# Optimization experiments

Measured on AMD Instinct MI355X. Metric: run time of the kernel, lower is better.

## Reference

```python
import jax, jax.numpy as jnp
import numpy as np

B, S, D, H = 4, 1024, 1024, 16
DK = D // H
NEG = -1e9


def setup_inputs() -> dict:
    key = jax.random.key(0)
    ks = jax.random.split(key, 14)
    sc = 1.0 / np.sqrt(D)
    inp = {
        "query": jax.random.normal(ks[0], (B, S, D), jnp.float32),
        "key": jax.random.normal(ks[1], (B, S, D), jnp.float32),
        "value": jax.random.normal(ks[2], (B, S, D), jnp.float32),
        "mask": jax.random.randint(ks[3], (B, S, S), 0, 2, jnp.int32),
        "group_prob": jax.random.uniform(ks[4], (B, S, S), jnp.float32),
        "Wq": jax.random.normal(ks[5], (D, D), jnp.float32) * sc,
        "bq": jnp.zeros((D,), jnp.float32),
        "Wk": jax.random.normal(ks[6], (D, D), jnp.float32) * sc,
        "bk": jnp.zeros((D,), jnp.float32),
        "Wv": jax.random.normal(ks[7], (D, D), jnp.float32) * sc,
        "bv": jnp.zeros((D,), jnp.float32),
        "Wo": jax.random.normal(ks[8], (D, D), jnp.float32) * sc,
        "bo": jnp.zeros((D,), jnp.float32),
    }
    return inp


def reference(query, key, value, mask, group_prob, Wq, bq, Wk, bk, Wv, bv, Wo, bo):
    # QKV projections, split heads: [B,S,D] -> [B,H,S,DK]
    def proj(x, W, b):
        return (x @ W.T + b).reshape(B, S, H, DK).transpose(0, 2, 1, 3)

    q = proj(query, Wq, bq)
    k = proj(key, Wk, bk)
    v = proj(value, Wv, bv)

    scores = jnp.einsum("bhqd,bhkd->bhqk", q, k) / jnp.sqrt(jnp.float32(DK))

    # group_prob branch: allowed where mask OR diagonal is nonzero
    diag = jnp.eye(S, dtype=jnp.int32)
    allowed = (mask[:, None, :, :] | diag[None, None, :, :]) != 0  # [B,1,S,S]
    scores = jnp.where(allowed, scores, NEG)

    p_attn = jax.nn.softmax(scores, axis=-1)
    p_attn = p_attn * group_prob[:, None, :, :]  # post-softmax group reweighting

    x = jnp.einsum("bhqk,bhkd->bhqd", p_attn, v)
    x = x.transpose(0, 2, 1, 3).reshape(B, S, D)
    return x @ Wo.T + bo
```

## Files before the change

kernel.cpp:

```cpp
#include <hip/hip_runtime.h>
#include <hip/hip_bf16.h>


typedef __attribute__((ext_vector_type(8))) __bf16 bf16x8;
typedef __attribute__((ext_vector_type(4))) float f32x4;
typedef __attribute__((ext_vector_type(8))) unsigned short u16x8;

#define GSTR 40

__device__ __forceinline__ bf16x8 lds_read8(const unsigned short* p) {
  bf16x8 r;
  __builtin_memcpy(&r, __builtin_assume_aligned(p, 16), 16);
  return r;
}
__device__ __forceinline__ void lds_write8(unsigned short* p, const void* v) {
  __builtin_memcpy(__builtin_assume_aligned(p, 16), v, 16);
}
__device__ __forceinline__ u16x8 cvt8h(const float4 a, const float4 b) {
  const float fv[8] = {a.x, a.y, a.z, a.w, b.x, b.y, b.z, b.w};
  union { u16x8 v; __bf16 e[8]; } hh;
#pragma unroll
  for (int i = 0; i < 8; ++i) hh.e[i] = (__bf16)fv[i];
  return hh.v;
}
__device__ __forceinline__ void cvt8hl(const float4 a, const float4 b, u16x8* hi, u16x8* lo) {
  const float fv[8] = {a.x, a.y, a.z, a.w, b.x, b.y, b.z, b.w};
  union { u16x8 v; __bf16 e[8]; } hh, ll;
#pragma unroll
  for (int i = 0; i < 8; ++i) {
    const __bf16 h = (__bf16)fv[i];
    hh.e[i] = h;
    ll.e[i] = (__bf16)(fv[i] - (float)h);
  }
  *hi = hh.v; *lo = ll.v;
}
__device__ __forceinline__ unsigned short bfbits(float f) {
  const __bf16 h = (__bf16)f;
  unsigned short u; __builtin_memcpy(&u, &h, 2); return u;
}

__global__ __launch_bounds__(256) void k_gemm_qkv(
    const float* __restrict__ X0, const float* __restrict__ X1, const float* __restrict__ X2,
    const float* __restrict__ W0, const float* __restrict__ W1, const float* __restrict__ W2,
    const float* __restrict__ B0, const float* __restrict__ B1, const float* __restrict__ B2,
    float* __restrict__ O0, float* __restrict__ O1, float* __restrict__ O2)
{
  const int z = blockIdx.z;
  const float* X = (z == 0) ? X0 : (z == 1) ? X1 : X2;
  const float* W = (z == 0) ? W0 : (z == 1) ? W1 : W2;
  const float* Bi = (z == 0) ? B0 : (z == 1) ? B1 : B2;
  float* O = (z == 0) ? O0 : (z == 1) ? O1 : O2;

  const int bid = blockIdx.x;
  const int swz = (bid & 7) * 64 + (bid >> 3);
  const int n0 = (swz & 15) * 64, m0 = (swz >> 4) * 128;

  __shared__ alignas(16) unsigned short Ah[128 * GSTR];
  __shared__ alignas(16) unsigned short Bh[64 * GSTR];
  const int tid = threadIdx.x, l = tid & 63, w = tid >> 6;
  const int wr = w >> 1, wc = w & 1;

  f32x4 acc[4][2];
#pragma unroll
  for (int i = 0; i < 4; ++i)
#pragma unroll
    for (int j = 0; j < 2; ++j) acc[i][j] = (f32x4){0.f, 0.f, 0.f, 0.f};

  const int arow = tid >> 1, ac0 = (tid & 1) * 16;
  const int brow = tid >> 2, bc0 = (tid & 3) * 8;
  const float* xsrc = X + (size_t)(m0 + arow) * 1024 + ac0;
  const float* wsrc = W + (size_t)(n0 + brow) * 1024 + bc0;

  float4 fx[4], fw[2];
#pragma unroll
  for (int i = 0; i < 4; ++i) fx[i] = *(const float4*)(xsrc + i * 4);
#pragma unroll
  for (int i = 0; i < 2; ++i) fw[i] = *(const float4*)(wsrc + i * 4);

  for (int kt = 0; kt < 32; ++kt) {
    u16x8 xh[2], wh1;
    xh[0] = cvt8h(fx[0], fx[1]);
    xh[1] = cvt8h(fx[2], fx[3]);
    wh1 = cvt8h(fw[0], fw[1]);
    if (kt < 31) {
      const float* nx = xsrc + (kt + 1) * 32;
      const float* nw = wsrc + (kt + 1) * 32;
#pragma unroll
      for (int i = 0; i < 4; ++i) fx[i] = *(const float4*)(nx + i * 4);
#pragma unroll
      for (int i = 0; i < 2; ++i) fw[i] = *(const float4*)(nw + i * 4);
    }
    __syncthreads();
    lds_write8(&Ah[arow * GSTR + ac0], &xh[0]);
    lds_write8(&Ah[arow * GSTR + ac0 + 8], &xh[1]);
    lds_write8(&Bh[brow * GSTR + bc0], &wh1);
    __syncthreads();

    bf16x8 ah[4], bh[2];
#pragma unroll
    for (int mf = 0; mf < 4; ++mf) {
      const int r = wr * 64 + mf * 16 + (l & 15);
      ah[mf] = lds_read8(&Ah[r * GSTR + (l >> 4) * 8]);
    }
#pragma unroll
    for (int nf = 0; nf < 2; ++nf) {
      const int r = wc * 32 + nf * 16 + (l & 15);
      bh[nf] = lds_read8(&Bh[r * GSTR + (l >> 4) * 8]);
    }
#pragma unroll
    for (int mf = 0; mf < 4; ++mf)
#pragma unroll
      for (int nf = 0; nf < 2; ++nf)
        acc[mf][nf] = __builtin_amdgcn_mfma_f32_16x16x32_bf16(ah[mf], bh[nf], acc[mf][nf], 0, 0, 0);
  }

#pragma unroll
  for (int nf = 0; nf < 2; ++nf) {
    const int col = n0 + wc * 32 + nf * 16 + (l & 15);
    const float bias = Bi[col];
#pragma unroll
    for (int mf = 0; mf < 4; ++mf) {
      const int rbase = m0 + wr * 64 + mf * 16 + (l >> 4) * 4;
#pragma unroll
      for (int j = 0; j < 4; ++j)
        O[(size_t)(rbase + j) * 1024 + col] = acc[mf][nf][j] + bias;
    }
  }
}

__global__ __launch_bounds__(256) void k_gemm_out(
    const float* __restrict__ X, const float* __restrict__ W,
    const float* __restrict__ Bi, float* __restrict__ Out)
{
  const int bid = blockIdx.x;
  const int swz = (bid & 7) * 128 + (bid >> 3);
  const int n0 = (swz & 15) * 64, m0 = (swz >> 4) * 64;

  __shared__ alignas(16) unsigned short Ah[64 * GSTR];
  __shared__ alignas(16) unsigned short Bh[64 * GSTR], Bl[64 * GSTR];
  const int tid = threadIdx.x, l = tid & 63, w = tid >> 6;
  const int wr = w >> 1, wc = w & 1;

  f32x4 acc[2][2];
#pragma unroll
  for (int i = 0; i < 2; ++i)
#pragma unroll
    for (int j = 0; j < 2; ++j) acc[i][j] = (f32x4){0.f, 0.f, 0.f, 0.f};

  const int srow = tid >> 2, sc0 = (tid & 3) * 8;
  const float* xsrc = X + (size_t)(m0 + srow) * 1024 + sc0;
  const float* wsrc = W + (size_t)(n0 + srow) * 1024 + sc0;

  float4 fx[2], fw[2];
#pragma unroll
  for (int i = 0; i < 2; ++i) {
    fx[i] = *(const float4*)(xsrc + i * 4);
    fw[i] = *(const float4*)(wsrc + i * 4);
  }

  for (int kt = 0; kt < 32; ++kt) {
    u16x8 xh, wh1, wl1;
    xh = cvt8h(fx[0], fx[1]);
    cvt8hl(fw[0], fw[1], &wh1, &wl1);
    if (kt < 31) {
      const float* nx = xsrc + (kt + 1) * 32;
      const float* nw = wsrc + (kt + 1) * 32;
#pragma unroll
      for (int i = 0; i < 2; ++i) {
        fx[i] = *(const float4*)(nx + i * 4);
        fw[i] = *(const float4*)(nw + i * 4);
      }
    }
    __syncthreads();
    lds_write8(&Ah[srow * GSTR + sc0], &xh);
    lds_write8(&Bh[srow * GSTR + sc0], &wh1);
    lds_write8(&Bl[srow * GSTR + sc0], &wl1);
    __syncthreads();

    bf16x8 ah[2], bh[2], bl[2];
#pragma unroll
    for (int mf = 0; mf < 2; ++mf) {
      const int r = wr * 32 + mf * 16 + (l & 15);
      ah[mf] = lds_read8(&Ah[r * GSTR + (l >> 4) * 8]);
    }
#pragma unroll
    for (int nf = 0; nf < 2; ++nf) {
      const int r = wc * 32 + nf * 16 + (l & 15);
      bh[nf] = lds_read8(&Bh[r * GSTR + (l >> 4) * 8]);
      bl[nf] = lds_read8(&Bl[r * GSTR + (l >> 4) * 8]);
    }
#pragma unroll
    for (int mf = 0; mf < 2; ++mf)
#pragma unroll
      for (int nf = 0; nf < 2; ++nf) {
        acc[mf][nf] = __builtin_amdgcn_mfma_f32_16x16x32_bf16(ah[mf], bh[nf], acc[mf][nf], 0, 0, 0);
        acc[mf][nf] = __builtin_amdgcn_mfma_f32_16x16x32_bf16(ah[mf], bl[nf], acc[mf][nf], 0, 0, 0);
      }
  }

#pragma unroll
  for (int nf = 0; nf < 2; ++nf) {
    const int col = n0 + wc * 32 + nf * 16 + (l & 15);
    const float bias = Bi[col];
#pragma unroll
    for (int mf = 0; mf < 2; ++mf) {
      const int rbase = m0 + wr * 32 + mf * 16 + (l >> 4) * 4;
#pragma unroll
      for (int j = 0; j < 4; ++j)
        Out[(size_t)(rbase + j) * 1024 + col] = acc[mf][nf][j] + bias;
    }
  }
}

__global__ __launch_bounds__(256) void k_attn(
    const float* Qp, const float* __restrict__ Kp, const float* __restrict__ Vp,
    const int* __restrict__ Mask, const float* __restrict__ Gp,
    float* Xo)
{
  const int h = blockIdx.x, qt = blockIdx.y, b = blockIdx.z;
  __shared__ alignas(16) unsigned short Kh[64 * 64], Vh[64 * 64], Ph[64 * 64];
  const int tid = threadIdx.x, l = tid & 63, w = tid >> 6;

  const float* kbase = Kp + (size_t)b * 1048576 + h * 64;
  const float* vbase = Vp + (size_t)b * 1048576 + h * 64;

  bf16x8 aq[2];
  {
    const int qrow = qt * 64 + w * 16 + (l & 15);
    const float* qp_ = Qp + ((size_t)(b * 1024 + qrow)) * 1024 + h * 64;
#pragma unroll
    for (int ks = 0; ks < 2; ++ks) {
      const float4 t0 = *(const float4*)(qp_ + ks * 32 + (l >> 4) * 8);
      const float4 t1 = *(const float4*)(qp_ + ks * 32 + (l >> 4) * 8 + 4);
      aq[ks] = (bf16x8)cvt8h(t0, t1);
    }
  }

  f32x4 accO[4];
#pragma unroll
  for (int nf = 0; nf < 4; ++nf) accO[nf] = (f32x4){0.f, 0.f, 0.f, 0.f};
  float zacc[4] = {0.f, 0.f, 0.f, 0.f};

  const int qloc0 = w * 16 + (l >> 4) * 4;
  const int qg0 = qt * 64 + qloc0;
  const int mcol = l & 15;

  const int krow = tid >> 2, kd0 = (tid & 3) * 16;
  const int kb4 = (tid & 15) * 4, db4 = (tid >> 4) * 4;

  float4 kreg[4], vreg[4];
  {
    const float* ks_ = kbase + (size_t)krow * 1024 + kd0;
#pragma unroll
    for (int i = 0; i < 4; ++i) kreg[i] = *(const float4*)(ks_ + i * 4);
    const float* vs_ = vbase + (size_t)kb4 * 1024 + db4;
#pragma unroll
    for (int i = 0; i < 4; ++i) vreg[i] = *(const float4*)(vs_ + (size_t)i * 1024);
  }

  for (int kt = 0; kt < 16; ++kt) {
    __syncthreads();

    int mk[4][4]; float gv[4][4];
#pragma unroll
    for (int nf = 0; nf < 4; ++nf) {
      const int kg = kt * 64 + nf * 16 + mcol;
#pragma unroll
      for (int j = 0; j < 4; ++j) {
        const size_t roff = ((size_t)(b * 1024 + qg0 + j)) << 10;
        mk[nf][j] = Mask[roff + kg];
        gv[nf][j] = Gp[roff + kg];
      }
    }

    {
      u16x8 h0 = cvt8h(kreg[0], kreg[1]);
      u16x8 h1 = cvt8h(kreg[2], kreg[3]);
      const int c0 = kd0 ^ ((krow & 7) << 3);
      const int c1 = (kd0 + 8) ^ ((krow & 7) << 3);
      lds_write8(&Kh[krow * 64 + c0], &h0);
      lds_write8(&Kh[krow * 64 + c1], &h1);
    }
    {
      const float col[4][4] = {{vreg[0].x, vreg[1].x, vreg[2].x, vreg[3].x},
                               {vreg[0].y, vreg[1].y, vreg[2].y, vreg[3].y},
                               {vreg[0].z, vreg[1].z, vreg[2].z, vreg[3].z},
                               {vreg[0].w, vreg[1].w, vreg[2].w, vreg[3].w}};
#pragma unroll
      for (int i = 0; i < 4; ++i) {
        const int d = db4 + i;
        union { __bf16 e[4]; unsigned long long v; } pk;
#pragma unroll
        for (int u = 0; u < 4; ++u) pk.e[u] = (__bf16)col[i][u];
        const int c = kb4 ^ ((d & 7) << 3);
        __builtin_memcpy(__builtin_assume_aligned(&Vh[d * 64 + c], 8), &pk.v, 8);
      }
    }
    if (kt < 15) {
      const float* ks_ = kbase + (size_t)((kt + 1) * 64 + krow) * 1024 + kd0;
#pragma unroll
      for (int i = 0; i < 4; ++i) kreg[i] = *(const float4*)(ks_ + i * 4);
      const float* vs_ = vbase + (size_t)((kt + 1) * 64 + kb4) * 1024 + db4;
#pragma unroll
      for (int i = 0; i < 4; ++i) vreg[i] = *(const float4*)(vs_ + (size_t)i * 1024);
    }
    __syncthreads();

#pragma unroll
    for (int nf = 0; nf < 4; ++nf) {
      f32x4 sacc = (f32x4){0.f, 0.f, 0.f, 0.f};
      const int kr = nf * 16 + (l & 15);
#pragma unroll
      for (int ks = 0; ks < 2; ++ks) {
        const int c = (ks * 32 + (l >> 4) * 8) ^ ((kr & 7) << 3);
        sacc = __builtin_amdgcn_mfma_f32_16x16x32_bf16(aq[ks], lds_read8(&Kh[kr * 64 + c]), sacc, 0, 0, 0);
      }
      const int kg = kt * 64 + nf * 16 + mcol;
#pragma unroll
      for (int j = 0; j < 4; ++j) {
        const int qg = qg0 + j;
        const int allowed = mk[nf][j] | (qg == kg);
        const float e = allowed ? exp2f(fmaf(sacc[j], 0.18033688f, -17.31234049f)) : 0.f;
        zacc[j] += e;
        const int qloc = qloc0 + j;
        Ph[qloc * 64 + ((nf * 16 + mcol) ^ ((qloc & 7) << 3))] = bfbits(e * gv[nf][j]);
      }
    }
    bf16x8 pah[2];
    {
      const int ar = w * 16 + (l & 15);
#pragma unroll
      for (int ks = 0; ks < 2; ++ks) {
        const int c = (ks * 32 + (l >> 4) * 8) ^ ((ar & 7) << 3);
        pah[ks] = lds_read8(&Ph[ar * 64 + c]);
      }
    }
#pragma unroll
    for (int nf = 0; nf < 4; ++nf) {
      const int dr = nf * 16 + (l & 15);
#pragma unroll
      for (int ks = 0; ks < 2; ++ks) {
        const int c = (ks * 32 + (l >> 4) * 8) ^ ((dr & 7) << 3);
        accO[nf] = __builtin_amdgcn_mfma_f32_16x16x32_bf16(pah[ks], lds_read8(&Vh[dr * 64 + c]), accO[nf], 0, 0, 0);
      }
    }
  }

#pragma unroll
  for (int j = 0; j < 4; ++j) {
#pragma unroll
    for (int off = 1; off < 16; off <<= 1) zacc[j] += __shfl_xor(zacc[j], off, 64);
  }
  float rz[4];
#pragma unroll
  for (int j = 0; j < 4; ++j) rz[j] = 1.f / zacc[j];

#pragma unroll
  for (int nf = 0; nf < 4; ++nf) {
    const int d = nf * 16 + (l & 15);
#pragma unroll
    for (int j = 0; j < 4; ++j) {
      const int qg = qg0 + j;
      Xo[((size_t)(b * 1024 + qg)) * 1024 + h * 64 + d] = accO[nf][j] * rz[j];
    }
  }
}

extern "C" void kernel_launch(void* const* d_in, const int* in_sizes, int n_in,
                              void* d_out, int out_size, void* d_ws, size_t ws_size,
                              hipStream_t stream) {
  const float* query = (const float*)d_in[0];
  const float* key_in = (const float*)d_in[1];
  const float* value = (const float*)d_in[2];
  const int* mask = (const int*)d_in[3];
  const float* gp = (const float*)d_in[4];
  const float* Wq = (const float*)d_in[5];
  const float* bq = (const float*)d_in[6];
  const float* Wk = (const float*)d_in[7];
  const float* bk = (const float*)d_in[8];
  const float* Wv = (const float*)d_in[9];
  const float* bv = (const float*)d_in[10];
  const float* Wo = (const float*)d_in[11];
  const float* bo = (const float*)d_in[12];
  float* out = (float*)d_out;

  float* kp = (float*)d_ws;
  float* vp = kp + 4194304;
  float* qp = vp + 4194304;
  float* xo = qp;

  hipLaunchKernelGGL(k_gemm_qkv, dim3(512, 1, 3), dim3(256), 0, stream,
                     query, key_in, value, Wq, Wk, Wv, bq, bk, bv, qp, kp, vp);
  hipLaunchKernelGGL(k_attn, dim3(16, 16, 4), dim3(256), 0, stream,
                     qp, kp, vp, mask, gp, xo);
  hipLaunchKernelGGL(k_gemm_out, dim3(1024), dim3(256), 0, stream,
                     xo, Wo, bo, out);
}
```

Measured before the change: 196.0 us.

## Store Q/K/V and attention output intermediates as bf16 with async K loads

The QKV projection now writes bf16 instead of fp32, and the attention kernel and output GEMM read bf16 directly. This halves intermediate memory traffic and removes the in-kernel conversions. The attention kernel also double-buffers K tiles in LDS using global_load_lds direct-to-LDS copies and restructures the mask/group-prob loads. The values were already rounded to bf16 before the MFMAs, so accuracy is essentially unchanged, though the attention output X is now stored in bf16.

Measured after the change: 182.1 us. -7.1%, faster.

```diff
diff --git a/kernel.cpp b/kernel.cpp
--- a/kernel.cpp
+++ b/kernel.cpp
@@ -1,6 +1,9 @@
 #include <hip/hip_runtime.h>
 #include <hip/hip_bf16.h>
 
+
+#define AS1q __attribute__((address_space(1)))
+#define AS3q __attribute__((address_space(3)))
 
 typedef __attribute__((ext_vector_type(8))) __bf16 bf16x8;
 typedef __attribute__((ext_vector_type(4))) float f32x4;
@@ -8,6 +11,9 @@
 
 #define GSTR 40
 
+__device__ __forceinline__ void gload_lds16(const void* g, void* l) {
+  __builtin_amdgcn_global_load_lds((const AS1q void*)g, (AS3q void*)l, 16, 0, 0);
+}
 __device__ __forceinline__ bf16x8 lds_read8(const unsigned short* p) {
   bf16x8 r;
   __builtin_memcpy(&r, __builtin_assume_aligned(p, 16), 16);
@@ -43,13 +49,14 @@
     const float* __restrict__ X0, const float* __restrict__ X1, const float* __restrict__ X2,
     const float* __restrict__ W0, const float* __restrict__ W1, const float* __restrict__ W2,
     const float* __restrict__ B0, const float* __restrict__ B1, const float* __restrict__ B2,
-    float* __restrict__ O0, float* __restrict__ O1, float* __restrict__ O2)
+    unsigned short* __restrict__ O0, unsigned short* __restrict__ O1,
+    unsigned short* __restrict__ O2)
 {
   const int z = blockIdx.z;
   const float* X = (z == 0) ? X0 : (z == 1) ? X1 : X2;
   const float* W = (z == 0) ? W0 : (z == 1) ? W1 : W2;
   const float* Bi = (z == 0) ? B0 : (z == 1) ? B1 : B2;
-  float* O = (z == 0) ? O0 : (z == 1) ? O1 : O2;
+  unsigned short* O = (z == 0) ? O0 : (z == 1) ? O1 : O2;
 
   const int bid = blockIdx.x;
   const int swz = (bid & 7) * 64 + (bid >> 3);
@@ -123,13 +130,13 @@
       const int rbase = m0 + wr * 64 + mf * 16 + (l >> 4) * 4;
 #pragma unroll
       for (int j = 0; j < 4; ++j)
-        O[(size_t)(rbase + j) * 1024 + col] = acc[mf][nf][j] + bias;
+        O[(size_t)(rbase + j) * 1024 + col] = bfbits(acc[mf][nf][j] + bias);
     }
   }
 }
 
 __global__ __launch_bounds__(256) void k_gemm_out(
-    const float* __restrict__ X, const float* __restrict__ W,
+    const unsigned short* __restrict__ X, const float* __restrict__ W,
     const float* __restrict__ Bi, float* __restrict__ Out)
 {
   const int bid = blockIdx.x;
@@ -148,31 +155,26 @@
     for (int j = 0; j < 2; ++j) acc[i][j] = (f32x4){0.f, 0.f, 0.f, 0.f};
 
   const int srow = tid >> 2, sc0 = (tid & 3) * 8;
-  const float* xsrc = X + (size_t)(m0 + srow) * 1024 + sc0;
+  const unsigned short* xsrc = X + (size_t)(m0 + srow) * 1024 + sc0;
   const float* wsrc = W + (size_t)(n0 + srow) * 1024 + sc0;
 
-  float4 fx[2], fw[2];
-#pragma unroll
-  for (int i = 0; i < 2; ++i) {
-    fx[i] = *(const float4*)(xsrc + i * 4);
-    fw[i] = *(const float4*)(wsrc + i * 4);
-  }
+  u16x8 xcur = *(const u16x8*)xsrc;
+  float4 fw[2];
+#pragma unroll
+  for (int i = 0; i < 2; ++i) fw[i] = *(const float4*)(wsrc + i * 4);
 
   for (int kt = 0; kt < 32; ++kt) {
-    u16x8 xh, wh1, wl1;
-    xh = cvt8h(fx[0], fx[1]);
+    const u16x8 xstage = xcur;
+    u16x8 wh1, wl1;
     cvt8hl(fw[0], fw[1], &wh1, &wl1);
     if (kt < 31) {
-      const float* nx = xsrc + (kt + 1) * 32;
+      xcur = *(const u16x8*)(xsrc + (kt + 1) * 32);
       const float* nw = wsrc + (kt + 1) * 32;
 #pragma unroll
-      for (int i = 0; i < 2; ++i) {
-        fx[i] = *(const float4*)(nx + i * 4);
-        fw[i] = *(const float4*)(nw + i * 4);
-      }
-    }
-    __syncthreads();
-    lds_write8(&Ah[srow * GSTR + sc0], &xh);
+      for (int i = 0; i < 2; ++i) fw[i] = *(const float4*)(nw + i * 4);
+    }
+    __syncthreads();
+    lds_write8(&Ah[srow * GSTR + sc0], &xstage);
     lds_write8(&Bh[srow * GSTR + sc0], &wh1);
     lds_write8(&Bl[srow * GSTR + sc0], &wl1);
     __syncthreads();
@@ -213,27 +215,26 @@
 }
 
 __global__ __launch_bounds__(256) void k_attn(
-    const float* Qp, const float* __restrict__ Kp, const float* __restrict__ Vp,
+    const unsigned short* Qh, const unsigned short* __restrict__ Kb,
+    const unsigned short* __restrict__ Vb,
     const int* __restrict__ Mask, const float* __restrict__ Gp,
-    float* Xo)
+    unsigned short* Xo)
 {
   const int h = blockIdx.x, qt = blockIdx.y, b = blockIdx.z;
-  __shared__ alignas(16) unsigned short Kh[64 * 64], Vh[64 * 64], Ph[64 * 64];
+  __shared__ alignas(16) unsigned short Kh[2][64 * 64];
+  __shared__ alignas(16) unsigned short Vh[64 * 64];
+  __shared__ alignas(16) unsigned short Ph[64 * 64];
   const int tid = threadIdx.x, l = tid & 63, w = tid >> 6;
 
-  const float* kbase = Kp + (size_t)b * 1048576 + h * 64;
-  const float* vbase = Vp + (size_t)b * 1048576 + h * 64;
+  const unsigned short* kb_ = Kb + (size_t)b * 1048576 + h * 64;
+  const unsigned short* vb_ = Vb + (size_t)b * 1048576 + h * 64;
 
   bf16x8 aq[2];
   {
     const int qrow = qt * 64 + w * 16 + (l & 15);
-    const float* qp_ = Qp + ((size_t)(b * 1024 + qrow)) * 1024 + h * 64;
-#pragma unroll
-    for (int ks = 0; ks < 2; ++ks) {
-      const float4 t0 = *(const float4*)(qp_ + ks * 32 + (l >> 4) * 8);
-      const float4 t1 = *(const float4*)(qp_ + ks * 32 + (l >> 4) * 8 + 4);
-      aq[ks] = (bf16x8)cvt8h(t0, t1);
-    }
+    const unsigned short* qp_ = Qh + ((size_t)(b * 1024 + qrow)) * 1024 + h * 64;
+    aq[0] = lds_read8  (qp_ + (l >> 4) * 8);
+    aq[1] = lds_read8(qp_ + 32 + (l >> 4) * 8);
   }
 
   f32x4 accO[4];
@@ -245,66 +246,56 @@
   const int qg0 = qt * 64 + qloc0;
   const int mcol = l & 15;
 
-  const int krow = tid >> 2, kd0 = (tid & 3) * 16;
+  const int srcg8 = (((l & 7) ^ (l >> 3))) * 8;
+  const int rowl = l >> 3;
+
   const int kb4 = (tid & 15) * 4, db4 = (tid >> 4) * 4;
 
-  float4 kreg[4], vreg[4];
-  {
-    const float* ks_ = kbase + (size_t)krow * 1024 + kd0;
-#pragma unroll
-    for (int i = 0; i < 4; ++i) kreg[i] = *(const float4*)(ks_ + i * 4);
-    const float* vs_ = vbase + (size_t)kb4 * 1024 + db4;
-#pragma unroll
-    for (int i = 0; i < 4; ++i) vreg[i] = *(const float4*)(vs_ + (size_t)i * 1024);
-  }
-
+  union U4 { unsigned int u[2]; unsigned short s[4]; };
+  U4 vr[4];
+
+#pragma unroll
+  for (int I = 0; I < 2; ++I)
+    gload_lds16(kb_ + (size_t)(I * 32 + w * 8 + rowl) * 1024 + srcg8,
+                &Kh[0][I * 2048 + w * 512]);
+#pragma unroll
+  for (int i = 0; i < 4; ++i)
+    __builtin_memcpy(&vr[i], vb_ + (size_t)(kb4 + i) * 1024 + db4, 8);
+
+  int buf = 0;
   for (int kt = 0; kt < 16; ++kt) {
     __syncthreads();
 
+#pragma unroll
+    for (int i = 0; i < 4; ++i) {
+      const int d = db4 + i;
+      union { unsigned short s[4]; unsigned long long v; } pk;
+#pragma unroll
+      for (int u = 0; u < 4; ++u) pk.s[u] = vr[u].s[i];
+      const int c = kb4 ^ ((d & 7) << 3);
+      __builtin_memcpy(__builtin_assume_aligned(&Vh[d * 64 + c], 8), &pk.v, 8);
+    }
+    __syncthreads();
+
+    if (kt < 15) {
+#pragma unroll
+      for (int I = 0; I < 2; ++I)
+        gload_lds16(kb_ + (size_t)((kt + 1) * 64 + I * 32 + w * 8 + rowl) * 1024 + srcg8,
+                    &Kh[buf ^ 1][I * 2048 + w * 512]);
+#pragma unroll
+      for (int i = 0; i < 4; ++i)
+        __builtin_memcpy(&vr[i], vb_ + (size_t)((kt + 1) * 64 + kb4 + i) * 1024 + db4, 8);
+    }
+
     int mk[4][4]; float gv[4][4];
 #pragma unroll
-    for (int nf = 0; nf < 4; ++nf) {
-      const int kg = kt * 64 + nf * 16 + mcol;
-#pragma unroll
-      for (int j = 0; j < 4; ++j) {
-        const size_t roff = ((size_t)(b * 1024 + qg0 + j)) << 10;
-        mk[nf][j] = Mask[roff + kg];
-        gv[nf][j] = Gp[roff + kg];
-      }
-    }
-
-    {
-      u16x8 h0 = cvt8h(kreg[0], kreg[1]);
-      u16x8 h1 = cvt8h(kreg[2], kreg[3]);
-      const int c0 = kd0 ^ ((krow & 7) << 3);
-      const int c1 = (kd0 + 8) ^ ((krow & 7) << 3);
-      lds_write8(&Kh[krow * 64 + c0], &h0);
-      lds_write8(&Kh[krow * 64 + c1], &h1);
-    }
-    {
-      const float col[4][4] = {{vreg[0].x, vreg[1].x, vreg[2].x, vreg[3].x},
-                               {vreg[0].y, vreg[1].y, vreg[2].y, vreg[3].y},
-                               {vreg[0].z, vreg[1].z, vreg[2].z, vreg[3].z},
-                               {vreg[0].w, vreg[1].w, vreg[2].w, vreg[3].w}};
-#pragma unroll
-      for (int i = 0; i < 4; ++i) {
-        const int d = db4 + i;
-        union { __bf16 e[4]; unsigned long long v; } pk;
-#pragma unroll
-        for (int u = 0; u < 4; ++u) pk.e[u] = (__bf16)col[i][u];
-        const int c = kb4 ^ ((d & 7) << 3);
-        __builtin_memcpy(__builtin_assume_aligned(&Vh[d * 64 + c], 8), &pk.v, 8);
-      }
-    }
-    if (kt < 15) {
-      const float* ks_ = kbase + (size_t)((kt + 1) * 64 + krow) * 1024 + kd0;
-#pragma unroll
-      for (int i = 0; i < 4; ++i) kreg[i] = *(const float4*)(ks_ + i * 4);
-      const float* vs_ = vbase + (size_t)((kt + 1) * 64 + kb4) * 1024 + db4;
-#pragma unroll
-      for (int i = 0; i < 4; ++i) vreg[i] = *(const float4*)(vs_ + (size_t)i * 1024);
-    }
-    __syncthreads();
+    for (int j = 0; j < 4; ++j) {
+      const size_t roff = ((size_t)(b * 1024 + qg0 + j)) << 10;
+      const int* mr = Mask + roff + kt * 64 + mcol;
+      const float* gr = Gp + roff + kt * 64 + mcol;
+#pragma unroll
+      for (int nf = 0; nf < 4; ++nf) { mk[nf][j] = mr[nf * 16]; gv[nf][j] = gr[nf * 16]; }
+    }
 
 #pragma unroll
     for (int nf = 0; nf < 4; ++nf) {
@@ -313,7 +304,7 @@
 #pragma unroll
       for (int ks = 0; ks < 2; ++ks) {
         const int c = (ks * 32 + (l >> 4) * 8) ^ ((kr & 7) << 3);
-        sacc = __builtin_amdgcn_mfma_f32_16x16x32_bf16(aq[ks], lds_read8(&Kh[kr * 64 + c]), sacc, 0, 0, 0);
+        sacc = __builtin_amdgcn_mfma_f32_16x16x32_bf16(aq[ks], lds_read8(&Kh[buf][kr * 64 + c]), sacc, 0, 0, 0);
       }
       const int kg = kt * 64 + nf * 16 + mcol;
 #pragma unroll
@@ -344,6 +335,7 @@
         accO[nf] = __builtin_amdgcn_mfma_f32_16x16x32_bf16(pah[ks], lds_read8(&Vh[dr * 64 + c]), accO[nf], 0, 0, 0);
       }
     }
+    buf ^= 1;
   }
 
 #pragma unroll
@@ -361,7 +353,7 @@
 #pragma unroll
     for (int j = 0; j < 4; ++j) {
       const int qg = qg0 + j;
-      Xo[((size_t)(b * 1024 + qg)) * 1024 + h * 64 + d] = accO[nf][j] * rz[j];
+      Xo[((size_t)(b * 1024 + qg)) * 1024 + h * 64 + d] = bfbits(accO[nf][j] * rz[j]);
     }
   }
 }
@@ -384,10 +376,10 @@
   const float* bo = (const float*)d_in[12];
   float* out = (float*)d_out;
 
-  float* kp = (float*)d_ws;
-  float* vp = kp + 4194304;
-  float* qp = vp + 4194304;
-  float* xo = qp;
+  unsigned short* kp = (unsigned short*)d_ws;
+  unsigned short* vp = kp + 4194304;
+  unsigned short* qp = vp + 4194304;
+  unsigned short* xo = qp;
 
   hipLaunchKernelGGL(k_gemm_qkv, dim3(512, 1, 3), dim3(256), 0, stream,
                      query, key_in, value, Wq, Wk, Wv, bq, bk, bv, qp, kp, vp);
```
